# Optimization experiments

Hardware: AMD Instinct MI355X
Metric: run time of the kernel (lower is better)

The kernel has to match this reference:

```python
import jax, jax.numpy as jnp
from jax import lax
import numpy as np

N_NODES = 8192
N_FEATURES = 1024
N_FILTRATIONS = 4
HIDDEN_DIM = 64
MAX_DEG = 8            # fixed out-degree used when generating edge_list
N_EDGES = N_NODES * MAX_DEG


def setup_inputs() -> dict:
    key = jax.random.key(0)
    ks = jax.random.split(key, 10)
    X = jax.random.normal(ks[0], (N_NODES, N_FEATURES), dtype=jnp.float32)
    # directed edge list, exactly MAX_DEG out-edges per node
    src = jnp.repeat(jnp.arange(N_NODES, dtype=jnp.int32), MAX_DEG)
    dst = jax.random.randint(ks[1], (N_EDGES,), 0, N_NODES, dtype=jnp.int32)
    edge_list = jnp.stack([src, dst], axis=0)
    # filtrations_nn: Linear(n_features,32) -> ReLU -> Linear(32,n_filtrations)
    W1 = jax.random.normal(ks[2], (32, N_FEATURES), dtype=jnp.float32) * 0.05
    b1 = jnp.zeros((32,), jnp.float32)
    W2 = jax.random.normal(ks[3], (N_FILTRATIONS, 32), dtype=jnp.float32) * 0.05
    b2 = jnp.zeros((N_FILTRATIONS,), jnp.float32)
    # deep sets: theta = Linear(2*n_filtrations, hidden), rho = Linear(1, n_features)
    Wt = jax.random.normal(ks[4], (HIDDEN_DIM, 2 * N_FILTRATIONS), dtype=jnp.float32) * 0.05
    bt = jnp.zeros((HIDDEN_DIM,), jnp.float32)
    Wr = jax.random.normal(ks[5], (N_FEATURES, 1), dtype=jnp.float32) * 0.05
    br = jnp.zeros((N_FEATURES,), jnp.float32)
    return {"X": X, "edge_list": edge_list, "W1": W1, "b1": b1, "W2": W2,
            "b2": b2, "Wt": Wt, "bt": bt, "Wr": Wr, "br": br}


def uf_find(parent, node):
    # chase parent pointers until a root (parent[v] == v)
    return lax.while_loop(lambda v: parent[v] != v, lambda v: parent[v], node)


def build_neighbor_table(edge_list, n_nodes, max_deg):
    # padded CSR-style neighbor table (n_nodes, max_deg), -1 = no edge
    src = edge_list[0].astype(jnp.int32)
    dst = edge_list[1].astype(jnp.int32)
    e = src.shape[0]
    order_e = jnp.argsort(src)  # stable
    src_s, dst_s = src[order_e], dst[order_e]
    counts = jnp.zeros(n_nodes, jnp.int32).at[src].add(1)
    offsets = jnp.concatenate([jnp.zeros(1, jnp.int32), jnp.cumsum(counts)[:-1].astype(jnp.int32)])
    slot = jnp.arange(e, dtype=jnp.int32) - offsets[src_s]
    return jnp.full((n_nodes, max_deg), -1, jnp.int32).at[src_s, slot].set(dst_s)


def persistence_dim0(values, nbr_table):
    """0-dim persistence via sequential union-find with elder rule.
    Row for sort-position j: (birth=j, death=step when the component born at j is absorbed).
    Returned indexed by node id (diagram[order[j]] = row j), matching the torch code."""
    n = values.shape[0]
    order = jnp.argsort(values).astype(jnp.int32)  # filtration order
    pos = jnp.zeros(n, jnp.int32).at[order].set(jnp.arange(n, dtype=jnp.int32))  # rank
    parent0 = jnp.arange(n, dtype=jnp.int32)
    deaths0 = jnp.zeros(n, jnp.float32)

    def step_fn(carry, sv):
        parent, deaths = carry
        s, vertex = sv
        nbrs = nbr_table[vertex]

        def edge_body(k, pc):
            parent, deaths = pc
            u = nbrs[k]
            u_c = jnp.maximum(u, 0)
            valid = (u >= 0) & (pos[u_c] <= s)  # neighbor already activated
            u_eff = jnp.where(valid, u_c, vertex)
            r1 = uf_find(parent, vertex)
            r2 = uf_find(parent, u_eff)
            parent = parent.at[vertex].set(r1).at[u_eff].set(r2)  # path compression
            merge = r1 != r2
            older_is_r1 = pos[r1] < pos[r2]
            absorbed = jnp.where(older_is_r1, r2, r1)   # younger root dies (elder rule)
            survivor = jnp.where(older_is_r1, r1, r2)
            parent = parent.at[absorbed].set(jnp.where(merge, survivor, absorbed))
            dp = pos[absorbed]
            deaths = deaths.at[dp].set(jnp.where(merge, s.astype(jnp.float32), deaths[dp]))
            return (parent, deaths)

        parent, deaths = lax.fori_loop(0, MAX_DEG, edge_body, (parent, deaths))
        return (parent, deaths), None

    (_, deaths), _ = lax.scan(step_fn, (parent0, deaths0),
                              (jnp.arange(n, dtype=jnp.int32), order))
    # finalize: undying components -> inf in the original; use finite cap n for numerics
    deaths = jnp.where(deaths == 0.0, jnp.float32(n), deaths)
    births = jnp.arange(n, dtype=jnp.float32)
    diag_sorted = jnp.stack([births, deaths], axis=1)  # (n, 2), row j = sort position j
    return jnp.zeros((n, 2), jnp.float32).at[order].set(diag_sorted)


def reference(X, edge_list, W1, b1, W2, b2, Wt, bt, Wr, br):
    n = X.shape[0]
    # filtrations_nn
    h = jax.nn.relu(X @ W1.T + b1)
    filt = h @ W2.T + b2                      # (n, n_filtrations)
    filt_ng = lax.stop_gradient(filt)         # diagram is piecewise constant in filt
    nbr_table = build_neighbor_table(edge_list, n, MAX_DEG)
    pds = [persistence_dim0(filt_ng[:, i], nbr_table) for i in range(N_FILTRATIONS)]
    pd = jnp.stack(pds, axis=0).transpose(1, 0, 2).reshape(n, 2 * N_FILTRATIONS)
    # DeepSetsAggregation(theta, rho) with index=zeros(hidden_dim), dim=1:
    theta = pd @ Wt.T + bt                    # (n, hidden)
    pooled = jnp.sum(theta, axis=1, keepdims=True)  # segment-sum of dim 1 into one bucket
    x_hat = pooled @ Wr.T + br                # (n, n_features)
    return X + x_hat
```

## Files before the change

kernel.cpp:

```cpp
#include <hip/hip_runtime.h>

#define N_NODES     8192
#define N_FEAT      1024
#define N_FILT      4
#define MAXDEG      8
#define BLK         256
#define NB          (N_NODES / BLK)

__global__ __launch_bounds__(256) void filt_kernel(
    const float* __restrict__ X, const float* __restrict__ W1,
    const float* __restrict__ b1, const float* __restrict__ W2,
    const float* __restrict__ b2, float* __restrict__ filtT)
{
    const int node = blockIdx.x * 8 + (threadIdx.x >> 5);
    const int h    = threadIdx.x & 31;
    const float* xr = X  + (size_t)node * N_FEAT;
    const float* wr = W1 + (size_t)h    * N_FEAT;
    float acc = 0.f;
    for (int j = 0; j < N_FEAT; j += 4) {
        float4 xv = *reinterpret_cast<const float4*>(xr + j);
        float4 wv = *reinterpret_cast<const float4*>(wr + j);
        acc += xv.x * wv.x + xv.y * wv.y + xv.z * wv.z + xv.w * wv.w;
    }
    float hv = fmaxf(acc + b1[h], 0.f);
    #pragma unroll
    for (int fo = 0; fo < N_FILT; ++fo) {
        float v = hv * W2[fo * 32 + h];
        for (int off = 16; off; off >>= 1) v += __shfl_xor(v, off, 32);
        if (h == 0) filtT[fo * N_NODES + node] = v + b2[fo];
    }
}

__global__ void wsum_kernel(const float* __restrict__ Wt,
                            const float* __restrict__ bt,
                            float* __restrict__ wsum)
{
    int t = threadIdx.x;
    if (t < 8) {
        float s = 0.f;
        for (int hh = 0; hh < 64; ++hh) s += Wt[hh * 8 + t];
        wsum[t] = s;
    } else if (t == 8) {
        float s = 0.f;
        for (int hh = 0; hh < 64; ++hh) s += bt[hh];
        wsum[8] = s;
    }
}

__global__ __launch_bounds__(256) void rank_partial_kernel(
    const float* __restrict__ filtT, unsigned short* __restrict__ partial)
{
    const int b  = blockIdx.x;
    const int f  = b >> 7;
    const int cs = (b >> 5) & 3;
    const int cv = b & 31;
    const int v  = (cv << 8) + threadIdx.x;
    const float myv = filtT[(f << 13) + v];

    __shared__ float4 tile[512];
    const float4* src = reinterpret_cast<const float4*>(filtT + (f << 13) + cs * 2048);
    for (int i = threadIdx.x; i < 512; i += 256) tile[i] = src[i];
    __syncthreads();

    int cnt = 0;
    const int ubase = cs * 2048;
    #pragma unroll 4
    for (int j = 0; j < 512; ++j) {
        float4 wv = tile[j];
        int u = ubase + j * 4;
        cnt += (wv.x < myv) || (wv.x == myv && (u + 0) < v);
        cnt += (wv.y < myv) || (wv.y == myv && (u + 1) < v);
        cnt += (wv.z < myv) || (wv.z == myv && (u + 2) < v);
        cnt += (wv.w < myv) || (wv.w == myv && (u + 3) < v);
    }
    partial[((f * 4 + cs) << 13) + v] = (unsigned short)cnt;
}

__global__ __launch_bounds__(256) void rank_final_kernel(
    const unsigned short* __restrict__ partial,
    unsigned short* __restrict__ pos16, unsigned short* __restrict__ order16)
{
    int g = blockIdx.x * 256 + threadIdx.x;
    int f = g >> 13, v = g & 8191;
    int r = (int)partial[((f * 4 + 0) << 13) + v]
          + (int)partial[((f * 4 + 1) << 13) + v]
          + (int)partial[((f * 4 + 2) << 13) + v]
          + (int)partial[((f * 4 + 3) << 13) + v];
    pos16[(f << 13) + v] = (unsigned short)r;
    order16[(f << 13) + r] = (unsigned short)v;
}

__global__ __launch_bounds__(256) void etable_kernel(
    const unsigned short* __restrict__ order16,
    const unsigned short* __restrict__ pos16,
    const int* __restrict__ edge_dst,
    unsigned short* __restrict__ et)
{
    const int f  = blockIdx.x >> 5;
    const int e0 = ((blockIdx.x & 31) << 11);
    for (int i = threadIdx.x; i < 2048; i += 256) {
        int e = e0 + i;
        int s = e >> 3, k = e & 7;
        int v = (int)order16[(f << 13) + s];
        int u = edge_dst[v * MAXDEG + k];
        int q = (int)pos16[(f << 13) + u];
        et[(size_t)f * (N_NODES * MAXDEG) + e] = (unsigned short)(q < s ? q : s);
    }
}

__device__ __forceinline__ int row8min(int v) {
    int t = min(v, __builtin_amdgcn_mov_dpp(v, 0xB1, 0xF, 0xF, true));
    t = min(t, __builtin_amdgcn_mov_dpp(t, 0x4E, 0xF, 0xF, true));
    t = min(t, __builtin_amdgcn_mov_dpp(t, 0x141, 0xF, 0xF, true));
    return t;
}

__device__ __forceinline__ void chase8(volatile unsigned int* vpd, int (&pk)[8]) {
    for (;;) {
        int qk[8];
        #pragma unroll
        for (int k = 0; k < 8; ++k) qk[k] = (int)(vpd[pk[k]] & 0xffffu);
        bool done = true;
        #pragma unroll
        for (int k = 0; k < 8; ++k) { done &= (qk[k] == pk[k]); pk[k] = qk[k]; }
        if (done) break;
    }
}

__global__ __launch_bounds__(256) void persist_kernel(
    const unsigned short* __restrict__ et,
    const unsigned short* __restrict__ pos16,
    unsigned short* __restrict__ death16)
{
    const int f    = blockIdx.x;
    const int tid  = threadIdx.x;
    const int lane = tid & 63;
    const int w    = tid >> 6;

    __shared__ unsigned int   s_pd[N_NODES];
    __shared__ unsigned short s_r16[2][BLK][8];
    __shared__ unsigned char  s_flag[2][BLK];
    __shared__ unsigned short s_list[2][BLK];
    __shared__ int s_wc[2][4];
    volatile unsigned int* vpd = s_pd;

    for (int v = tid; v < N_NODES; v += 256) s_pd[v] = (unsigned)v;
    __syncthreads();

    const unsigned short* etf = et + (size_t)f * (N_NODES * MAXDEG);

    for (int it = 0; it <= NB; ++it) {
        const int buf = it & 1;

        if (w == 0) {
            if (it > 0) {
                const int pbuf = (it - 1) & 1;
                const int plo  = (it - 1) * BLK;
                const int total = s_wc[pbuf][0] + s_wc[pbuf][1]
                                + s_wc[pbuf][2] + s_wc[pbuf][3];
                if (total > 0) {
                    int t_cur = (int)s_list[pbuf][0];
                    int p_cur = (int)s_r16[pbuf][t_cur][lane & 7];
                    for (int i = 0; i < total; ++i) {
                        int nidx  = (i + 1 < total) ? (i + 1) : i;
                        int t_nxt = (int)s_list[pbuf][nidx];
                        int p_nxt = (int)s_r16[pbuf][t_nxt][lane & 7];
                        const int sv = plo + t_cur;
                        int p = p_cur;
                        for (;;) {
                            int q = (int)(vpd[p] & 0xffffu);
                            if (__all(q == p)) break;
                            p = q;
                        }
                        int m = row8min(p);
                        if (lane < 8 && p != m)
                            vpd[p] = (unsigned)m | ((unsigned)sv << 16);
                        t_cur = t_nxt; p_cur = p_nxt;
                    }
                }
            }
        } else if (it < NB) {
            const int lo = it * BLK;
            const int h  = tid - 64;
            #pragma unroll
            for (int rep = 0; rep < 2; ++rep) {
                const int sl = (rep == 0) ? h : (192 + h);
                if (rep == 1 && h >= 64) break;
                const int s = lo + sl;
                uint4 raw = *reinterpret_cast<const uint4*>(etf + (size_t)s * 8);
                int e8[8];
                e8[0] = raw.x & 0xffff; e8[1] = raw.x >> 16;
                e8[2] = raw.y & 0xffff; e8[3] = raw.y >> 16;
                e8[4] = raw.z & 0xffff; e8[5] = raw.z >> 16;
                e8[6] = raw.w & 0xffff; e8[7] = raw.w >> 16;
                int pk[8];
                #pragma unroll
                for (int k = 0; k < 8; ++k) pk[k] = e8[k];
                chase8(vpd, pk);
                int first = -1; bool same = true;
                #pragma unroll
                for (int k = 0; k < 8; ++k) {
                    if (e8[k] == s) continue;
                    if (first < 0) first = pk[k];
                    else same &= (pk[k] == first);
                }
                if (first < 0) {
                    s_flag[buf][sl] = 0;
                } else if (same) {
                    vpd[s] = (unsigned)first | ((unsigned)s << 16);
                    s_flag[buf][sl] = 0;
                } else {
                    s_flag[buf][sl] = 2;
                    #pragma unroll
                    for (int k = 0; k < 8; ++k)
                        s_r16[buf][sl][k] = (unsigned short)pk[k];
                }
            }
        }
        __syncthreads();

        bool impure = false;
        int  within = 0;
        if (it < NB) {
            const int sl = tid;
            const int s  = it * BLK + sl;
            if (s_flag[buf][sl] == 2) {
                int pk[8];
                #pragma unroll
                for (int k = 0; k < 8; ++k) pk[k] = (int)s_r16[buf][sl][k];
                chase8(vpd, pk);
                int first = -1; bool same = true; int m = pk[0];
                #pragma unroll
                for (int k = 0; k < 8; ++k) {
                    m = min(m, pk[k]);
                    if (pk[k] == s) continue;
                    if (first < 0) first = pk[k];
                    else same &= (pk[k] == first);
                }
                if (same) {
                    vpd[s] = (unsigned)first | ((unsigned)s << 16);
                } else {
                    impure = true;
                    #pragma unroll
                    for (int k = 0; k < 8; ++k)
                        s_r16[buf][sl][k] = (unsigned short)pk[k];
                    vpd[s] = (unsigned)m | ((unsigned)s << 16);
                }
            }
        }
        unsigned long long bal = __ballot(impure);
        within = __popcll(bal & ((1ull << lane) - 1ull));
        if (it < NB && lane == 0) s_wc[buf][w] = __popcll(bal);
        __syncthreads();
        if (it < NB && impure) {
            int base = 0;
            #pragma unroll
            for (int i = 0; i < 4; ++i) { if (i < w) base += s_wc[buf][i]; }
            s_list[buf][base + within] = (unsigned short)tid;
        }
        __syncthreads();
    }

    for (int n = tid; n < N_NODES; n += 256) {
        int p = (int)pos16[(f << 13) + n];
        int d = (int)(s_pd[p] >> 16);
        death16[(f << 13) + n] = (unsigned short)(d ? d : N_NODES);
    }
}

__global__ __launch_bounds__(256) void out_kernel(
    const float* __restrict__ X, const float* __restrict__ Wr,
    const float* __restrict__ br,
    const unsigned short* __restrict__ pos16,
    const unsigned short* __restrict__ death16,
    const float* __restrict__ wsum,
    float* __restrict__ out)
{
    const int node = blockIdx.x;
    float pl = wsum[8];
    #pragma unroll
    for (int i = 0; i < N_FILT; ++i) {
        pl += (float)pos16[(i << 13) + node]   * wsum[2 * i + 0]
            + (float)death16[(i << 13) + node] * wsum[2 * i + 1];
    }
    const int fb = threadIdx.x * 4;
    const float4 xv = *reinterpret_cast<const float4*>(X + (size_t)node * N_FEAT + fb);
    const float4 wv = *reinterpret_cast<const float4*>(Wr + fb);
    const float4 bv = *reinterpret_cast<const float4*>(br + fb);
    float4 o;
    o.x = xv.x + pl * wv.x + bv.x;
    o.y = xv.y + pl * wv.y + bv.y;
    o.z = xv.z + pl * wv.z + bv.z;
    o.w = xv.w + pl * wv.w + bv.w;
    *reinterpret_cast<float4*>(out + (size_t)node * N_FEAT + fb) = o;
}

extern "C" void kernel_launch(void* const* d_in, const int* in_sizes, int n_in,
                              void* d_out, int out_size, void* d_ws, size_t ws_size,
                              hipStream_t stream) {
    const float* X  = (const float*)d_in[0];
    const int* edge = (const int*)d_in[1];
    const float* W1 = (const float*)d_in[2];
    const float* b1 = (const float*)d_in[3];
    const float* W2 = (const float*)d_in[4];
    const float* b2 = (const float*)d_in[5];
    const float* Wt = (const float*)d_in[6];
    const float* bt = (const float*)d_in[7];
    const float* Wr = (const float*)d_in[8];
    const float* br = (const float*)d_in[9];

    const int* edge_dst = edge + N_NODES * MAXDEG;

    char* wsb = (char*)d_ws;
    float*          filtT   = (float*)(wsb);
    unsigned short* pos16   = (unsigned short*)(wsb + 131072);
    unsigned short* order16 = (unsigned short*)(wsb + 196608);
    unsigned short* death16 = (unsigned short*)(wsb + 196608);
    unsigned short* partial = (unsigned short*)(wsb + 262144);
    unsigned short* et      = (unsigned short*)(wsb + 262144);
    float*          wsum    = (float*)(wsb + 786432);

    hipLaunchKernelGGL(filt_kernel,  dim3(N_NODES / 8), dim3(256), 0, stream,
                       X, W1, b1, W2, b2, filtT);
    hipLaunchKernelGGL(wsum_kernel,  dim3(1), dim3(64), 0, stream, Wt, bt, wsum);
    hipLaunchKernelGGL(rank_partial_kernel, dim3(512), dim3(256), 0, stream,
                       filtT, partial);
    hipLaunchKernelGGL(rank_final_kernel, dim3(128), dim3(256), 0, stream,
                       partial, pos16, order16);
    hipLaunchKernelGGL(etable_kernel, dim3(4 * 32), dim3(256), 0, stream,
                       order16, pos16, edge_dst, et);
    hipLaunchKernelGGL(persist_kernel, dim3(N_FILT), dim3(256), 0, stream,
                       et, pos16, death16);
    hipLaunchKernelGGL(out_kernel,   dim3(N_NODES), dim3(256), 0, stream,
                       X, Wr, br, pos16, death16, wsum, (float*)d_out);
}
```

Baseline: 646.3 us.

## Batch eight impure nodes per wavefront in serial union phase and mask resolved chases

The serial merge phase in wave 0 used to process impure nodes one at a time with 8 active lanes. It now loads up to eight nodes at once, one per 8-lane group, and chases all their roots in parallel. It then applies the unions in order, re-chasing only when an earlier union in the batch actually killed a component. The chase8 helper also stops re-reading neighbours whose root has already been found. The aim is to cut the latency of the sequential critical path, at the cost of more complex control flow and extra re-chases when kills are common.

```diff
diff --git a/kernel.cpp b/kernel.cpp
--- a/kernel.cpp
+++ b/kernel.cpp
@@ -115,15 +115,19 @@
     return t;
 }
 
-__device__ __forceinline__ void chase8(volatile unsigned int* vpd, int (&pk)[8]) {
+__device__ __forceinline__ void chase8m(volatile unsigned int* vpd, int (&pk)[8]) {
+    unsigned msk = 0;
     for (;;) {
-        int qk[8];
+        bool all = true;
         #pragma unroll
-        for (int k = 0; k < 8; ++k) qk[k] = (int)(vpd[pk[k]] & 0xffffu);
-        bool done = true;
-        #pragma unroll
-        for (int k = 0; k < 8; ++k) { done &= (qk[k] == pk[k]); pk[k] = qk[k]; }
-        if (done) break;
+        for (int k = 0; k < 8; ++k) {
+            if (!(msk & (1u << k))) {
+                int q = (int)(vpd[pk[k]] & 0xffffu);
+                if (q == pk[k]) msk |= (1u << k);
+                else { pk[k] = q; all = false; }
+            }
+        }
+        if (all) break;
     }
 }
 
@@ -158,24 +162,34 @@
                 const int plo  = (it - 1) * BLK;
                 const int total = s_wc[pbuf][0] + s_wc[pbuf][1]
                                 + s_wc[pbuf][2] + s_wc[pbuf][3];
-                if (total > 0) {
-                    int t_cur = (int)s_list[pbuf][0];
-                    int p_cur = (int)s_r16[pbuf][t_cur][lane & 7];
-                    for (int i = 0; i < total; ++i) {
-                        int nidx  = (i + 1 < total) ? (i + 1) : i;
-                        int t_nxt = (int)s_list[pbuf][nidx];
-                        int p_nxt = (int)s_r16[pbuf][t_nxt][lane & 7];
-                        const int sv = plo + t_cur;
-                        int p = p_cur;
-                        for (;;) {
-                            int q = (int)(vpd[p] & 0xffffu);
-                            if (__all(q == p)) break;
-                            p = q;
+                const int g    = lane >> 3;
+                const int slot = lane & 7;
+                for (int base = 0; base < total; base += 8) {
+                    int idx = base + g;
+                    if (idx >= total) idx = total - 1;
+                    const int t = (int)s_list[pbuf][idx];
+                    int p = (int)s_r16[pbuf][t][slot];
+                    for (;;) {
+                        int q = (int)(vpd[p] & 0xffffu);
+                        if (__all(q == p)) break;
+                        p = q;
+                    }
+                    const int gmax = (total - base < 8) ? (total - base) : 8;
+                    bool kprev = false;
+                    for (int gg = 0; gg < gmax; ++gg) {
+                        if (kprev) {
+                            for (;;) {
+                                int q = (int)(vpd[p] & 0xffffu);
+                                if (__all(q == p)) break;
+                                p = q;
+                            }
                         }
                         int m = row8min(p);
-                        if (lane < 8 && p != m)
-                            vpd[p] = (unsigned)m | ((unsigned)sv << 16);
-                        t_cur = t_nxt; p_cur = p_nxt;
+                        const bool ing  = (g == gg);
+                        const bool kill = ing && (p != m);
+                        kprev = (__ballot(kill) != 0ull);
+                        if (kill)
+                            vpd[p] = (unsigned)m | ((unsigned)(plo + t) << 16);
                     }
                 }
             }
@@ -196,7 +210,7 @@
                 int pk[8];
                 #pragma unroll
                 for (int k = 0; k < 8; ++k) pk[k] = e8[k];
-                chase8(vpd, pk);
+                chase8m(vpd, pk);
                 int first = -1; bool same = true;
                 #pragma unroll
                 for (int k = 0; k < 8; ++k) {
@@ -220,7 +234,6 @@
         __syncthreads();
 
         bool impure = false;
-        int  within = 0;
         if (it < NB) {
             const int sl = tid;
             const int s  = it * BLK + sl;
@@ -228,7 +241,7 @@
                 int pk[8];
                 #pragma unroll
                 for (int k = 0; k < 8; ++k) pk[k] = (int)s_r16[buf][sl][k];
-                chase8(vpd, pk);
+                chase8m(vpd, pk);
                 int first = -1; bool same = true; int m = pk[0];
                 #pragma unroll
                 for (int k = 0; k < 8; ++k) {
@@ -249,7 +262,7 @@
             }
         }
         unsigned long long bal = __ballot(impure);
-        within = __popcll(bal & ((1ull << lane) - 1ull));
+        int within = __popcll(bal & ((1ull << lane) - 1ull));
         if (it < NB && lane == 0) s_wc[buf][w] = __popcll(bal);
         __syncthreads();
         if (it < NB && impure) {
```

Result: slower. 767.5 us (+18.8%).
